# Performance work log

Measured on AMD Instinct MI355X. Metric: run time of the kernel, lower is better.

## Reference

```python
import jax, jax.numpy as jnp
import numpy as np

R = 4  # search_radius


def conv3(x, w, b):
    # 3x3 conv, padding=1 (SAME), NCHW / OIHW
    y = jax.lax.conv_general_dilated(x, w, window_strides=(1, 1), padding='SAME',
                                     dimension_numbers=('NCHW', 'OIHW', 'NCHW'))
    return y + b[None, :, None, None]


def bilinear_border(img, x, y):
    # torch F.grid_sample(mode='bilinear', padding_mode='border', align_corners=True)
    # img: (B,C,H,W); x,y: (B,H,W) unnormalized pixel coords
    B, C, H, W = img.shape
    x = jnp.clip(x, 0.0, W - 1.0)
    y = jnp.clip(y, 0.0, H - 1.0)
    x0 = jnp.floor(x)
    y0 = jnp.floor(y)
    x0i = x0.astype(jnp.int32)
    y0i = y0.astype(jnp.int32)
    x1i = jnp.minimum(x0i + 1, W - 1)
    y1i = jnp.minimum(y0i + 1, H - 1)
    wx = (x - x0)[..., None]
    wy = (y - y0)[..., None]
    imgt = jnp.transpose(img, (0, 2, 3, 1))  # (B,H,W,C)
    b = jnp.arange(B)[:, None, None]
    v00 = imgt[b, y0i, x0i]
    v01 = imgt[b, y0i, x1i]
    v10 = imgt[b, y1i, x0i]
    v11 = imgt[b, y1i, x1i]
    out = (v00 * (1 - wx) + v01 * wx) * (1 - wy) + (v10 * (1 - wx) + v11 * wx) * wy
    return jnp.transpose(out, (0, 3, 1, 2))


def _forward(feat1, feat2, initial_flow,
             fW1, fb1, fW2, fb2, fW3, fb3,
             rW1, rb1, rW2, rb2, rW3, rb3, rW4, rb4):
    relu = jax.nn.relu

    def extract(x):
        x = relu(conv3(x, fW1, fb1))
        x = relu(conv3(x, fW2, fb2))
        return relu(conv3(x, fW3, fb3))  # (B, 32, H, W)

    f1 = extract(feat1)
    f2 = extract(feat2)
    B, C, H, W = f1.shape
    yy, xx = jnp.meshgrid(jnp.arange(H, dtype=jnp.float32),
                          jnp.arange(W, dtype=jnp.float32), indexing='ij')
    # warp feat2 by initial flow; align_corners=True normalization cancels -> pixel coords + flow
    f2w = bilinear_border(f2, xx[None] + initial_flow[:, 0], yy[None] + initial_flow[:, 1])
    # search offsets, same order as search_grid.view(2,-1).t(): (dx, dy) row-major over (dy rows)
    coords = jnp.arange(-R, R + 1, dtype=jnp.float32)
    gy, gx = jnp.meshgrid(coords, coords, indexing='ij')
    offs = jnp.stack([gx.reshape(-1), gy.reshape(-1)], axis=1)  # (81, 2)
    xb = jnp.broadcast_to(xx[None], (B, H, W))
    yb = jnp.broadcast_to(yy[None], (B, H, W))

    def cost_fn(off):
        shifted = bilinear_border(f2w, xb + off[0], yb + off[1])
        return jnp.sum(f1 * shifted, axis=1)  # (B,H,W)

    cv = jnp.transpose(jax.lax.map(cost_fn, offs), (1, 0, 2, 3))  # (B,81,H,W)
    h = jnp.concatenate([cv, initial_flow], axis=1)  # (B,83,H,W)
    h = relu(conv3(h, rW1, rb1))
    h = relu(conv3(h, rW2, rb2))
    h = relu(conv3(h, rW3, rb3))
    return initial_flow + conv3(h, rW4, rb4)


def setup_inputs():
    key = jax.random.key(0)
    ks = jax.random.split(key, 12)
    B, H, W = 2, 256, 448
    FC = 64
    CV = (2 * R + 1) ** 2  # 81
    s = 0.05
    d = {}
    d['feat1'] = jax.random.normal(ks[0], (B, 3, H, W), jnp.float32)
    d['feat2'] = jax.random.normal(ks[1], (B, 3, H, W), jnp.float32)
    d['initial_flow'] = jax.random.normal(ks[2], (B, 2, H, W), jnp.float32)
    d['fW1'] = jax.random.normal(ks[3], (FC, 3, 3, 3), jnp.float32) * s
    d['fb1'] = jnp.zeros((FC,), jnp.float32)
    d['fW2'] = jax.random.normal(ks[4], (FC, FC, 3, 3), jnp.float32) * s
    d['fb2'] = jnp.zeros((FC,), jnp.float32)
    d['fW3'] = jax.random.normal(ks[5], (FC // 2, FC, 3, 3), jnp.float32) * s
    d['fb3'] = jnp.zeros((FC // 2,), jnp.float32)
    d['rW1'] = jax.random.normal(ks[6], (128, CV + 2, 3, 3), jnp.float32) * s
    d['rb1'] = jnp.zeros((128,), jnp.float32)
    d['rW2'] = jax.random.normal(ks[7], (128, 128, 3, 3), jnp.float32) * s
    d['rb2'] = jnp.zeros((128,), jnp.float32)
    d['rW3'] = jax.random.normal(ks[8], (64, 128, 3, 3), jnp.float32) * s
    d['rb3'] = jnp.zeros((64,), jnp.float32)
    d['rW4'] = jax.random.normal(ks[9], (2, 64, 3, 3), jnp.float32) * s
    d['rb4'] = jnp.zeros((2,), jnp.float32)
    return d


def reference(feat1, feat2, initial_flow,
              fW1, fb1, fW2, fb2, fW3, fb3,
              rW1, rb1, rW2, rb2, rW3, rb3, rW4, rb4):
    return _forward(feat1, feat2, initial_flow,
                    fW1, fb1, fW2, fb2, fW3, fb3,
                    rW1, rb1, rW2, rb2, rW3, rb3, rW4, rb4)
```

## Files before the change

kernel.cpp:

```cpp
#include <hip/hip_runtime.h>

#define HH 256
#define WW 448
#define HW (HH * WW)

typedef short bf16x8 __attribute__((ext_vector_type(8)));
typedef float f32x4 __attribute__((ext_vector_type(4)));
typedef unsigned int uint32;
typedef unsigned short ushort;

__device__ __forceinline__ ushort f2bf(float f) {
    uint32 u = __float_as_uint(f);
    u += 0x7fffu + ((u >> 16) & 1u);
    return (ushort)(u >> 16);
}

__device__ __forceinline__ void pack_one(
    int i, const float* __restrict__ w, ushort* __restrict__ wp,
    int CinReal, int CinPad, int Cout)
{
    int total = 9 * CinPad * Cout;
    if (i >= total) return;
    int ci = i & 31;
    int rest = i >> 5;
    int n = rest % Cout;
    int rest2 = rest / Cout;
    int KC = CinPad / 32;
    int kc = rest2 % KC;
    int tap = rest2 / KC;
    int cin = kc * 32 + ci;
    float v = (cin < CinReal) ? w[((size_t)n * CinReal + cin) * 9 + tap] : 0.f;
    wp[i] = f2bf(v);
}

__global__ __launch_bounds__(256) void pack_all_k(
    const float* fW2, const float* fW3, const float* rW1,
    const float* rW2, const float* rW3,
    ushort* wp2, ushort* wp3, ushort* wpr1, ushort* wpr2, ushort* wpr3)
{
    int i = blockIdx.x * 256 + threadIdx.x;
    pack_one(i, fW2, wp2, 64, 64, 64);
    pack_one(i, fW3, wp3, 64, 64, 32);
    pack_one(i, rW1, wpr1, 83, 96, 128);
    pack_one(i, rW2, wpr2, 128, 128, 128);
    pack_one(i, rW3, wpr3, 128, 128, 64);
}

template <int CIN, int COUT, int RELU>
__global__ __launch_bounds__(256, 4) void convmfma_k(
    const ushort* __restrict__ in, const ushort* __restrict__ wp,
    const float* __restrict__ bias, ushort* __restrict__ out,
    long inStride, long outStride)
{
    constexpr int KC = CIN / 32;
    constexpr int NPH = (CIN + 63) / 64;
    constexpr int CS = 72;
    constexpr int NG = (COUT >= 64) ? 4 : 2;
    constexpr int WN = (COUT / 16) / NG;
    constexpr int MG = 4 / NG;
    constexpr int WM = 8 / MG;

    __shared__ __align__(16) ushort lds[180 * CS];

    const int tid = threadIdx.x;
    const int x0 = blockIdx.x * 16;
    const int y0 = blockIdx.y * 8;
    in += (size_t)blockIdx.z * inStride;
    out += (size_t)blockIdx.z * outStride;

    const int wv = tid >> 6;
    const int lane = tid & 63;
    const int m = lane & 15;
    const int quad = lane >> 4;
    const int mbase = (wv % MG) * WM;
    const int nbase = (wv / MG) * WN * 16;

    const ushort* ldsA = lds + (mbase * 18 + m) * CS + quad * 8;
    const ushort* wpB = wp + ((size_t)nbase + m) * 32 + quad * 8;

    f32x4 acc[WM][WN];
#pragma unroll
    for (int t = 0; t < WM; ++t)
#pragma unroll
        for (int u = 0; u < WN; ++u)
            acc[t][u] = (f32x4){0.f, 0.f, 0.f, 0.f};

#pragma unroll 1
    for (int ph = 0; ph < NPH; ++ph) {
        const int C = (CIN - ph * 64 >= 64) ? 64 : (CIN - ph * 64);
        const int sh = (C == 64) ? 3 : 2;
        const int ch8 = C >> 3;

        if (ph) __syncthreads();
        for (int i = tid; i < 180 * ch8; i += 256) {
            int p = i >> sh, c8 = i & (ch8 - 1);
            int ry = p / 18, rx = p - ry * 18;
            int gy = y0 + ry - 1, gx = x0 + rx - 1;
            float4 v = make_float4(0.f, 0.f, 0.f, 0.f);
            if (gy >= 0 && gy < HH && gx >= 0 && gx < WW)
                v = *(const float4*)(in + ((size_t)gy * WW + gx) * CIN + ph * 64 + c8 * 8);
            *(float4*)(lds + p * CS + c8 * 8) = v;
        }
        __syncthreads();

        const int KCc = C / 32;
        const ushort* wpP = wpB + (size_t)(ph * 2) * COUT * 32;
#pragma unroll 1
        for (int tap = 0; tap < 9; ++tap) {
            const int ky = tap / 3;
            const int kx = tap - 3 * ky;
            const ushort* wpT = wpP + (size_t)tap * KC * COUT * 32;
#pragma unroll
            for (int kc = 0; kc < 2; ++kc) {
                if (kc >= KCc) break;
                bf16x8 b[WN];
#pragma unroll
                for (int u = 0; u < WN; ++u)
                    b[u] = *(const bf16x8*)(wpT + ((size_t)kc * COUT + u * 16) * 32);
#pragma unroll
                for (int th = 0; th < WM / 4; ++th) {
                    bf16x8 a[4];
#pragma unroll
                    for (int t4 = 0; t4 < 4; ++t4)
                        a[t4] = *(const bf16x8*)(ldsA +
                                ((th * 4 + t4 + ky) * 18 + kx) * CS + kc * 32);
#pragma unroll
                    for (int t4 = 0; t4 < 4; ++t4)
#pragma unroll
                        for (int u = 0; u < WN; ++u)
                            acc[th * 4 + t4][u] =
                                __builtin_amdgcn_mfma_f32_16x16x32_bf16(
                                    a[t4], b[u], acc[th * 4 + t4][u], 0, 0, 0);
                }
            }
        }
    }

#pragma unroll
    for (int u = 0; u < WN; ++u) {
        const int n = nbase + u * 16 + m;
        const float bs = bias[n];
#pragma unroll
        for (int t = 0; t < WM; ++t) {
            const int y = y0 + mbase + t;
#pragma unroll
            for (int r = 0; r < 4; ++r) {
                const int x = x0 + quad * 4 + r;
                float v = acc[t][u][r] + bs;
                if (RELU) v = fmaxf(v, 0.f);
                out[((size_t)y * WW + x) * COUT + n] = f2bf(v);
            }
        }
    }
}

__global__ __launch_bounds__(256) void fconv1_k(
    const float* __restrict__ in, const float* __restrict__ w,
    const float* __restrict__ bias, ushort* __restrict__ out,
    long inStride, long outStride)
{
    __shared__ float wl[1728];
    __shared__ float patch[3][4][18];
    const int tid = threadIdx.x;
    const int x0 = blockIdx.x * 16, y0 = blockIdx.y * 2;
    in += (size_t)blockIdx.z * inStride;
    out += (size_t)blockIdx.z * outStride;
    for (int i = tid; i < 1728; i += 256) wl[i] = w[i];
    for (int i = tid; i < 216; i += 256) {
        int ci = i / 72;
        int r = (i - ci * 72) / 18;
        int c = i - ci * 72 - r * 18;
        int gy = y0 + r - 1, gx = x0 + c - 1;
        patch[ci][r][c] = (gy >= 0 && gy < HH && gx >= 0 && gx < WW)
                              ? in[(size_t)ci * HW + gy * WW + gx] : 0.f;
    }
    __syncthreads();
    const int g = tid & 7;
    const int p = tid >> 3;
    const int py = p >> 4, px = p & 15;
    float acc[8];
#pragma unroll
    for (int j = 0; j < 8; ++j) acc[j] = bias[g * 8 + j];
#pragma unroll
    for (int ci = 0; ci < 3; ++ci)
#pragma unroll
        for (int k = 0; k < 9; ++k) {
            const int ky = k / 3, kx = k - 3 * ky;
            const float v = patch[ci][py + ky][px + kx];
#pragma unroll
            for (int j = 0; j < 8; ++j)
                acc[j] = fmaf(v, wl[(g * 8 + j) * 27 + ci * 9 + k], acc[j]);
        }
    ushort ov[8];
#pragma unroll
    for (int j = 0; j < 8; ++j) ov[j] = f2bf(fmaxf(acc[j], 0.f));
    const int y = y0 + py, x = x0 + px;
    *(float4*)(out + ((size_t)y * WW + x) * 64 + g * 8) = *(const float4*)ov;
}

__global__ __launch_bounds__(256) void warp_k(
    const ushort* __restrict__ f2, const float* __restrict__ flow,
    ushort* __restrict__ outp, long fStride, long flowStride, long oStride)
{
    int idx = blockIdx.x * 256 + threadIdx.x;
    if (idx >= HW) return;
    f2 += (size_t)blockIdx.y * fStride;
    flow += (size_t)blockIdx.y * flowStride;
    outp += (size_t)blockIdx.y * oStride;
    int y = idx / WW, x = idx - y * WW;
    float px_ = (float)x + flow[idx];
    float py_ = (float)y + flow[idx + HW];
    px_ = fminf(fmaxf(px_, 0.f), (float)(WW - 1));
    py_ = fminf(fmaxf(py_, 0.f), (float)(HH - 1));
    float fx0 = floorf(px_), fy0 = floorf(py_);
    int xi0 = (int)fx0, yi0 = (int)fy0;
    int xi1 = min(xi0 + 1, WW - 1), yi1 = min(yi0 + 1, HH - 1);
    float wx = px_ - fx0, wy = py_ - fy0;
    float w00 = (1.f - wx) * (1.f - wy), w01 = wx * (1.f - wy);
    float w10 = (1.f - wx) * wy, w11 = wx * wy;

    const uint32* a = (const uint32*)(f2 + ((size_t)yi0 * WW + xi0) * 32);
    const uint32* b = (const uint32*)(f2 + ((size_t)yi0 * WW + xi1) * 32);
    const uint32* c = (const uint32*)(f2 + ((size_t)yi1 * WW + xi0) * 32);
    const uint32* d = (const uint32*)(f2 + ((size_t)yi1 * WW + xi1) * 32);
    uint32 ov[16];
#pragma unroll
    for (int i = 0; i < 16; ++i) {
        uint32 wa = a[i], wb = b[i], wc = c[i], wd = d[i];
        float lo = __uint_as_float(wa << 16) * w00 + __uint_as_float(wb << 16) * w01 +
                   __uint_as_float(wc << 16) * w10 + __uint_as_float(wd << 16) * w11;
        float hi = __uint_as_float(wa & 0xffff0000u) * w00 + __uint_as_float(wb & 0xffff0000u) * w01 +
                   __uint_as_float(wc & 0xffff0000u) * w10 + __uint_as_float(wd & 0xffff0000u) * w11;
        ov[i] = ((uint32)f2bf(hi) << 16) | f2bf(lo);
    }
    uint32* o = (uint32*)(outp + (size_t)idx * 32);
#pragma unroll
    for (int i = 0; i < 16; ++i) o[i] = ov[i];
}

__global__ __launch_bounds__(128) void cost_tile_k(
    const ushort* __restrict__ f1, const ushort* __restrict__ f2w,
    const float* __restrict__ flow, ushort* __restrict__ hb,
    long aStride, long flowStride)
{
    __shared__ ushort ldsG[16 * 24 * 36];
    const int tid = threadIdx.x;
    const int x0 = blockIdx.x * 16;
    const int y0 = blockIdx.y * 8;
    f1 += (size_t)blockIdx.z * aStride;
    f2w += (size_t)blockIdx.z * aStride;
    hb += (size_t)blockIdx.z * aStride;
    flow += (size_t)blockIdx.z * flowStride;

#pragma unroll
    for (int i = 0; i < 24; ++i) {
        int idx = i * 128 + tid;
        int hp = idx >> 3;
        int c4 = idx & 7;
        int ry = hp / 24, rx = hp - ry * 24;
        int gy = min(max(y0 + ry - 4, 0), HH - 1);
        int gx = min(max(x0 + rx - 4, 0), WW - 1);
        *(uint2*)(ldsG + hp * 36 + c4 * 4) =
            *(const uint2*)(f2w + ((size_t)gy * WW + gx) * 32 + c4 * 4);
    }
    __syncthreads();

    const int tyy = tid >> 4, txx = tid & 15;
    const int px = (y0 + tyy) * WW + (x0 + txx);

    float f[32];
    const uint2* fp = (const uint2*)(f1 + (size_t)px * 32);
#pragma unroll
    for (int j = 0; j < 8; ++j) {
        uint2 w = fp[j];
        f[4 * j + 0] = __uint_as_float(w.x << 16);
        f[4 * j + 1] = __uint_as_float(w.x & 0xffff0000u);
        f[4 * j + 2] = __uint_as_float(w.y << 16);
        f[4 * j + 3] = __uint_as_float(w.y & 0xffff0000u);
    }

    ushort* hq = hb + (size_t)px * 96;
    for (int dyi = 0; dyi < 9; ++dyi) {
        const ushort* gp0 = ldsG + ((tyy + dyi) * 24 + txx) * 36;
#pragma unroll
        for (int dxi = 0; dxi < 9; ++dxi) {
            const ushort* gp = gp0 + dxi * 36;
            float s = 0.f;
#pragma unroll
            for (int j = 0; j < 8; ++j) {
                uint2 g = *(const uint2*)(gp + j * 4);
                s = fmaf(f[4 * j + 0], __uint_as_float(g.x << 16), s);
                s = fmaf(f[4 * j + 1], __uint_as_float(g.x & 0xffff0000u), s);
                s = fmaf(f[4 * j + 2], __uint_as_float(g.y << 16), s);
                s = fmaf(f[4 * j + 3], __uint_as_float(g.y & 0xffff0000u), s);
            }
            hq[dyi * 9 + dxi] = f2bf(s);
        }
    }
    hq[81] = f2bf(flow[px]);
    hq[82] = f2bf(flow[px + HW]);
#pragma unroll
    for (int c = 83; c < 96; ++c) hq[c] = 0;
}

__global__ __launch_bounds__(256) void rconv4_k(
    const ushort* __restrict__ in, const float* __restrict__ w,
    const float* __restrict__ bias, const float* __restrict__ flow,
    float* __restrict__ out, long inStride, long ioStride)
{
    __shared__ float wl[1152];
    for (int i = threadIdx.x; i < 1152; i += 256) wl[i] = w[i];
    __syncthreads();
    in += (size_t)blockIdx.y * inStride;
    flow += (size_t)blockIdx.y * ioStride;
    out += (size_t)blockIdx.y * ioStride;
    int px = blockIdx.x * 256 + threadIdx.x;
    if (px >= HW) return;
    int y = px / WW, x = px - y * WW;
    float a0 = bias[0], a1 = bias[1];
    for (int ky = 0; ky < 3; ++ky) {
        int gy = y + ky - 1;
        if (gy < 0 || gy >= HH) continue;
        for (int kx = 0; kx < 3; ++kx) {
            int gx = x + kx - 1;
            if (gx < 0 || gx >= WW) continue;
            const uint32* p = (const uint32*)(in + ((size_t)gy * WW + gx) * 64);
            int tap = ky * 3 + kx;
#pragma unroll
            for (int i = 0; i < 32; ++i) {
                uint32 wv = p[i];
                float lo = __uint_as_float(wv << 16);
                float hi = __uint_as_float(wv & 0xffff0000u);
                a0 = fmaf(lo, wl[(2 * i) * 9 + tap], a0);
                a0 = fmaf(hi, wl[(2 * i + 1) * 9 + tap], a0);
                a1 = fmaf(lo, wl[576 + (2 * i) * 9 + tap], a1);
                a1 = fmaf(hi, wl[576 + (2 * i + 1) * 9 + tap], a1);
            }
        }
    }
    out[px] = flow[px] + a0;
    out[px + HW] = flow[px + HW] + a1;
}

extern "C" void kernel_launch(void* const* d_in, const int* in_sizes, int n_in,
                              void* d_out, int out_size, void* d_ws, size_t ws_size,
                              hipStream_t stream)
{
    (void)in_sizes; (void)n_in; (void)out_size;
    const float* feat1 = (const float*)d_in[0];
    const float* feat2 = (const float*)d_in[1];
    const float* iflow = (const float*)d_in[2];
    const float* fW1 = (const float*)d_in[3];  const float* fb1 = (const float*)d_in[4];
    const float* fW2 = (const float*)d_in[5];  const float* fb2 = (const float*)d_in[6];
    const float* fW3 = (const float*)d_in[7];  const float* fb3 = (const float*)d_in[8];
    const float* rW1 = (const float*)d_in[9];  const float* rb1 = (const float*)d_in[10];
    const float* rW2 = (const float*)d_in[11]; const float* rb2 = (const float*)d_in[12];
    const float* rW3 = (const float*)d_in[13]; const float* rb3 = (const float*)d_in[14];
    const float* rW4 = (const float*)d_in[15]; const float* rb4 = (const float*)d_in[16];
    float* out = (float*)d_out;

    const size_t P = (size_t)HW;
    const size_t WTOT = (size_t)9 * (64 * 64 + 64 * 32 + 96 * 128 + 128 * 128 + 128 * 64);
    const size_t ARENA = 320 * P;
    ushort* ws0 = (ushort*)d_ws;
    ushort* wp2  = ws0;
    ushort* wp3  = wp2 + 9 * 64 * 64;
    ushort* wpr1 = wp3 + 9 * 64 * 32;
    ushort* wpr2 = wpr1 + 9 * 96 * 128;
    ushort* wpr3 = wpr2 + 9 * 128 * 128;
    ushort* arena = ws0 + WTOT;

    const bool merged = ws_size >= (WTOT + 2 * ARENA) * sizeof(ushort);
    const int nb = merged ? 2 : 1;
    const int nloop = merged ? 1 : 2;
    const long aS = merged ? (long)ARENA : 0;
    const long s3 = merged ? (long)(3 * P) : 0;
    const long s2 = merged ? (long)(2 * P) : 0;

    ushort* X0  = arena;
    ushort* X1  = X0 + 64 * P;
    ushort* F1  = X1 + 64 * P;
    ushort* F2  = F1 + 32 * P;
    ushort* F2W = F2 + 32 * P;
    ushort* Hb  = F2W + 32 * P;
    ushort* R1  = X0;
    ushort* R2  = F2W;
    ushort* R3  = F1;

    const dim3 blk(256);
    pack_all_k<<<dim3((9 * 128 * 128 + 255) / 256), blk, 0, stream>>>(
        fW2, fW3, rW1, rW2, rW3, wp2, wp3, wpr1, wpr2, wpr3);

    const dim3 gConv(WW / 16, HH / 8, nb);
    const dim3 gF1(WW / 16, HH / 2, nb);
    const dim3 gCost(WW / 16, HH / 8, nb);
    const int gPix = (HW + 255) / 256;

    for (int lb = 0; lb < nloop; ++lb) {
        const float* f1in = feat1 + (size_t)lb * 3 * P;
        const float* f2in = feat2 + (size_t)lb * 3 * P;
        const float* flw  = iflow + (size_t)lb * 2 * P;
        float* outb = out + (size_t)lb * 2 * P;

        fconv1_k<<<gF1, blk, 0, stream>>>(f2in, fW1, fb1, X0, s3, aS);
        convmfma_k<64, 64, 1><<<gConv, blk, 0, stream>>>(X0, wp2, fb2, X1, aS, aS);
        convmfma_k<64, 32, 1><<<gConv, blk, 0, stream>>>(X1, wp3, fb3, F2, aS, aS);
        warp_k<<<dim3(gPix, nb), blk, 0, stream>>>(F2, flw, F2W, aS, s2, aS);

        fconv1_k<<<gF1, blk, 0, stream>>>(f1in, fW1, fb1, X0, s3, aS);
        convmfma_k<64, 64, 1><<<gConv, blk, 0, stream>>>(X0, wp2, fb2, X1, aS, aS);
        convmfma_k<64, 32, 1><<<gConv, blk, 0, stream>>>(X1, wp3, fb3, F1, aS, aS);

        cost_tile_k<<<gCost, dim3(128), 0, stream>>>(F1, F2W, flw, Hb, aS, s2);

        convmfma_k<96, 128, 1><<<gConv, blk, 0, stream>>>(Hb, wpr1, rb1, R1, aS, aS);
        convmfma_k<128, 128, 1><<<gConv, blk, 0, stream>>>(R1, wpr2, rb2, R2, aS, aS);
        convmfma_k<128, 64, 1><<<gConv, blk, 0, stream>>>(R2, wpr3, rb3, R3, aS, aS);
        rconv4_k<<<dim3(gPix, nb), blk, 0, stream>>>(R3, rW4, rb4, flw, outb, aS, s2);
    }
}
```

Before: 529.8 us.

## Compute correlation cost volume with MFMA instead of scalar FMA

Replaces the LDS-tiled scalar dot-product cost kernel with an MFMA version. Each wave handles one 16-pixel row segment and issues two 16x16x32 bf16 MFMAs per vertical offset against a 32-wide strip of warped features, keeping only the diagonal band of 9 horizontal offsets. This moves the 81x32 dot products onto matrix cores, but drops shared-memory reuse, wastes most of each MFMA output on entries outside the band, and writes the results as scattered 2-byte stores.

Measured after the change: 506.2 us. 4.4% less time.

```diff
diff --git a/kernel.cpp b/kernel.cpp
--- a/kernel.cpp
+++ b/kernel.cpp
@@ -238,69 +238,59 @@
     for (int i = 0; i < 16; ++i) o[i] = ov[i];
 }
 
-__global__ __launch_bounds__(128) void cost_tile_k(
+__global__ __launch_bounds__(256) void cost_mfma_k(
     const ushort* __restrict__ f1, const ushort* __restrict__ f2w,
     const float* __restrict__ flow, ushort* __restrict__ hb,
     long aStride, long flowStride)
 {
-    __shared__ ushort ldsG[16 * 24 * 36];
     const int tid = threadIdx.x;
+    const int wv = tid >> 6;
+    const int lane = tid & 63;
+    const int c = lane & 15;
+    const int quad = lane >> 4;
     const int x0 = blockIdx.x * 16;
-    const int y0 = blockIdx.y * 8;
+    const int y = blockIdx.y * 4 + wv;
     f1 += (size_t)blockIdx.z * aStride;
     f2w += (size_t)blockIdx.z * aStride;
     hb += (size_t)blockIdx.z * aStride;
     flow += (size_t)blockIdx.z * flowStride;
 
-#pragma unroll
-    for (int i = 0; i < 24; ++i) {
-        int idx = i * 128 + tid;
-        int hp = idx >> 3;
-        int c4 = idx & 7;
-        int ry = hp / 24, rx = hp - ry * 24;
-        int gy = min(max(y0 + ry - 4, 0), HH - 1);
-        int gx = min(max(x0 + rx - 4, 0), WW - 1);
-        *(uint2*)(ldsG + hp * 36 + c4 * 4) =
-            *(const uint2*)(f2w + ((size_t)gy * WW + gx) * 32 + c4 * 4);
-    }
-    __syncthreads();
-
-    const int tyy = tid >> 4, txx = tid & 15;
-    const int px = (y0 + tyy) * WW + (x0 + txx);
-
-    float f[32];
-    const uint2* fp = (const uint2*)(f1 + (size_t)px * 32);
-#pragma unroll
-    for (int j = 0; j < 8; ++j) {
-        uint2 w = fp[j];
-        f[4 * j + 0] = __uint_as_float(w.x << 16);
-        f[4 * j + 1] = __uint_as_float(w.x & 0xffff0000u);
-        f[4 * j + 2] = __uint_as_float(w.y << 16);
-        f[4 * j + 3] = __uint_as_float(w.y & 0xffff0000u);
-    }
-
-    ushort* hq = hb + (size_t)px * 96;
+    const bf16x8 a = *(const bf16x8*)(f1 + ((size_t)y * WW + x0 + c) * 32 + quad * 8);
+
+    const int xc0 = min(max(x0 - 4 + c, 0), WW - 1);
+    const int xc1 = min(max(x0 + 12 + c, 0), WW - 1);
+
+    ushort* hrow = hb + ((size_t)y * WW + x0) * 96;
+
+#pragma unroll 1
     for (int dyi = 0; dyi < 9; ++dyi) {
-        const ushort* gp0 = ldsG + ((tyy + dyi) * 24 + txx) * 36;
-#pragma unroll
-        for (int dxi = 0; dxi < 9; ++dxi) {
-            const ushort* gp = gp0 + dxi * 36;
-            float s = 0.f;
-#pragma unroll
-            for (int j = 0; j < 8; ++j) {
-                uint2 g = *(const uint2*)(gp + j * 4);
-                s = fmaf(f[4 * j + 0], __uint_as_float(g.x << 16), s);
-                s = fmaf(f[4 * j + 1], __uint_as_float(g.x & 0xffff0000u), s);
-                s = fmaf(f[4 * j + 2], __uint_as_float(g.y << 16), s);
-                s = fmaf(f[4 * j + 3], __uint_as_float(g.y & 0xffff0000u), s);
-            }
-            hq[dyi * 9 + dxi] = f2bf(s);
-        }
-    }
-    hq[81] = f2bf(flow[px]);
-    hq[82] = f2bf(flow[px + HW]);
-#pragma unroll
-    for (int c = 83; c < 96; ++c) hq[c] = 0;
+        const int ys = min(max(y + dyi - 4, 0), HH - 1);
+        const bf16x8 b0 = *(const bf16x8*)(f2w + ((size_t)ys * WW + xc0) * 32 + quad * 8);
+        const bf16x8 b1 = *(const bf16x8*)(f2w + ((size_t)ys * WW + xc1) * 32 + quad * 8);
+        f32x4 s0 = __builtin_amdgcn_mfma_f32_16x16x32_bf16(
+            a, b0, (f32x4){0.f, 0.f, 0.f, 0.f}, 0, 0, 0);
+        f32x4 s1 = __builtin_amdgcn_mfma_f32_16x16x32_bf16(
+            a, b1, (f32x4){0.f, 0.f, 0.f, 0.f}, 0, 0, 0);
+
+        ushort* hq = hrow + dyi * 9;
+#pragma unroll
+        for (int r = 0; r < 4; ++r) {
+            const int m = quad * 4 + r;
+            const int d0 = c - m;
+            const int d1 = c + 16 - m;
+            if (d0 >= 0 && d0 <= 8) hq[(size_t)m * 96 + d0] = f2bf(s0[r]);
+            if (d1 <= 8) hq[(size_t)m * 96 + d1] = f2bf(s1[r]);
+        }
+    }
+
+    if (lane < 16) {
+        const int px = y * WW + x0 + lane;
+        ushort* hq = hb + (size_t)px * 96;
+        hq[81] = f2bf(flow[px]);
+        hq[82] = f2bf(flow[px + HW]);
+#pragma unroll
+        for (int ch = 83; ch < 96; ++ch) hq[ch] = 0;
+    }
 }
 
 __global__ __launch_bounds__(256) void rconv4_k(
@@ -393,7 +383,7 @@
 
     const dim3 gConv(WW / 16, HH / 8, nb);
     const dim3 gF1(WW / 16, HH / 2, nb);
-    const dim3 gCost(WW / 16, HH / 8, nb);
+    const dim3 gCost(WW / 16, HH / 4, nb);
     const int gPix = (HW + 255) / 256;
 
     for (int lb = 0; lb < nloop; ++lb) {
@@ -411,7 +401,7 @@
         convmfma_k<64, 64, 1><<<gConv, blk, 0, stream>>>(X0, wp2, fb2, X1, aS, aS);
         convmfma_k<64, 32, 1><<<gConv, blk, 0, stream>>>(X1, wp3, fb3, F1, aS, aS);
 
-        cost_tile_k<<<gCost, dim3(128), 0, stream>>>(F1, F2W, flw, Hb, aS, s2);
+        cost_mfma_k<<<gCost, blk, 0, stream>>>(F1, F2W, flw, Hb, aS, s2);
 
         convmfma_k<96, 128, 1><<<gConv, blk, 0, stream>>>(Hb, wpr1, rb1, R1, aS, aS);
         convmfma_k<128, 128, 1><<<gConv, blk, 0, stream>>>(R1, wpr2, rb2, R2, aS, aS);
```
